# Optimization experiments

Measured on AMD Instinct MI355X. Metric: run time of the kernel, lower is better.

Reference implementation:

```python
import jax, jax.numpy as jnp
import numpy as np

N, B, T, F_IN, H1, H2 = 69, 32, 1024, 8, 32, 16


def cal_adj_norm(adj):
    # adj_norm = D^-1/2 (A + I) D^-1/2
    n = adj.shape[0]
    adj_ = adj + jnp.eye(n, dtype=adj.dtype)
    d = jnp.sum(adj_, axis=1)
    d_is = d ** -0.5
    return adj_ * d_is[:, None] * d_is[None, :]


def setup_inputs() -> dict:
    key = jax.random.key(0)
    k1, k2, k3, k4 = jax.random.split(key, 4)
    x = jax.random.normal(k1, (N, B, T, F_IN), dtype=jnp.float32)
    a = jax.random.uniform(k2, (N, N), dtype=jnp.float32)
    adj = ((a + a.T) > 1.4).astype(jnp.float32)
    W1 = jax.random.normal(k3, (F_IN, H1), dtype=jnp.float32)
    W2 = jax.random.normal(k4, (H1, H2), dtype=jnp.float32)
    return {"x": x, "adj": adj, "W1": W1, "W2": W2}


def reference(x, adj, W1, W2):
    adj_n = cal_adj_norm(adj)                      # [N, N]
    xb = jnp.transpose(x, (1, 2, 0, 3))            # [B, T, N, F_in]
    # layer 1: relu( adj_n @ x @ W1 ), batched over (B, T)
    h = jax.nn.relu(jnp.einsum('nm,btmf->btnf', adj_n, xb) @ W1)   # [B, T, N, H1]
    # layer 2: sigmoid( adj_n @ h @ W2 )
    out = jax.nn.sigmoid(jnp.einsum('nm,btmf->btnf', adj_n, h) @ W2)  # [B, T, N, H2]
    return out
```

## Files before the change

### kernel.cpp

```cpp
#include <hip/hip_runtime.h>
#include <math.h>

#define N_NODES 69
#define MP      80
#define KP      96
#define BT_TOTAL 32768
#define F_IN    8
#define H1      32
#define H2      16

#define TBT     8
#define BLOCK   256

#define XPITCH  68
#define ZPITCH  136
#define RSTRIDE 72
#define RROWS   576

typedef __attribute__((ext_vector_type(8))) short bf16x8;
typedef __attribute__((ext_vector_type(4))) float f32x4;

__device__ __forceinline__ unsigned short f2bf(float f) {
    unsigned u = __float_as_uint(f);
    return (unsigned short)((u + 0x7FFFu + ((u >> 16) & 1u)) >> 16);
}
__device__ __forceinline__ float bf2f(unsigned short h) {
    return __uint_as_float(((unsigned)h) << 16);
}

__global__ void setup_kernel(const float* __restrict__ adj,
                             const float* __restrict__ W1,
                             const float* __restrict__ W2,
                             unsigned short* __restrict__ adjh,
                             unsigned short* __restrict__ adjl,
                             unsigned short* __restrict__ W1p,
                             unsigned short* __restrict__ W2p)
{
    __shared__ float dinv[N_NODES];
    const int tid = threadIdx.x;
    if (tid < N_NODES) {
        float s = 1.0f;
        for (int j = 0; j < N_NODES; ++j) s += adj[tid * N_NODES + j];
        dinv[tid] = rsqrtf(s);
    }
    __syncthreads();
    for (int idx = tid; idx < MP * KP; idx += BLOCK) {
        const int n = idx / KP, m = idx % KP;
        float v = 0.0f;
        if (n < N_NODES && m < N_NODES) {
            float a = adj[n * N_NODES + m] + (n == m ? 1.0f : 0.0f);
            v = a * dinv[n] * dinv[m];
        }
        unsigned short h = f2bf(v);
        adjh[idx] = h;
        adjl[idx] = f2bf(v - bf2f(h));
    }
    for (int i = tid; i < 2 * 64 * F_IN; i += BLOCK) {
        const int nt = i >> 9;
        const int ln = (i >> 3) & 63;
        const int j  = i & 7;
        const int q = ln >> 4, l = ln & 15;
        float v = (q == 0) ? W1[j * H1 + nt * 16 + l] : 0.0f;
        W1p[i] = f2bf(v);
    }
    for (int i = tid; i < 64 * F_IN; i += BLOCK) {
        const int ln = i >> 3, j = i & 7;
        const int q = ln >> 4, l = ln & 15;
        W2p[i] = f2bf(W2[(q * 8 + j) * H2 + l]);
    }
}

__global__ __launch_bounds__(BLOCK, 4) void gcn_kernel(
    const float* __restrict__ x,
    const unsigned short* __restrict__ adjh,
    const unsigned short* __restrict__ adjl,
    const unsigned short* __restrict__ W1p,
    const unsigned short* __restrict__ W2p,
    float* __restrict__ out)
{
    __shared__ unsigned short U_s[KP * ZPITCH];
    __shared__ unsigned short Y1_s[RROWS * F_IN];
    __shared__ unsigned short Hb_s[4][16 * H1];

    const int tid  = threadIdx.x;
    const int lane = tid & 63;
    const int wv   = tid >> 6;
    const int quad = lane >> 4;
    const int l16  = lane & 15;
    const int bt0  = blockIdx.x * TBT;

    unsigned short* Xhi = U_s;
    unsigned short* Xlo = U_s + KP * XPITCH;

    for (int i = tid; i < N_NODES * 16; i += BLOCK) {
        const int m = i >> 4, c4 = i & 15;
        const float4 v = ((const float4*)x)[(size_t)m * (BT_TOTAL * 2) + bt0 * 2 + c4];
        unsigned short h0 = f2bf(v.x), h1 = f2bf(v.y), h2 = f2bf(v.z), h3 = f2bf(v.w);
        uint2 hi2 = make_uint2((unsigned)h0 | ((unsigned)h1 << 16),
                               (unsigned)h2 | ((unsigned)h3 << 16));
        unsigned short g0 = f2bf(v.x - bf2f(h0)), g1 = f2bf(v.y - bf2f(h1));
        unsigned short g2 = f2bf(v.z - bf2f(h2)), g3 = f2bf(v.w - bf2f(h3));
        uint2 lo2 = make_uint2((unsigned)g0 | ((unsigned)g1 << 16),
                               (unsigned)g2 | ((unsigned)g3 << 16));
        *(uint2*)((char*)Xhi + 2 * (m * XPITCH + 4 * c4)) = hi2;
        *(uint2*)((char*)Xlo + 2 * (m * XPITCH + 4 * c4)) = lo2;
    }
    for (int i = tid; i < 27 * 34; i += BLOCK) {
        const int row = N_NODES + i / 34, w = i % 34;
        ((unsigned*)Xhi)[row * 34 + w] = 0u;
        ((unsigned*)Xlo)[row * 34 + w] = 0u;
    }
    __syncthreads();

    const bf16x8 w1f0 = *(const bf16x8*)&W1p[lane * 8];
    const bf16x8 w1f1 = *(const bf16x8*)&W1p[(64 + lane) * 8];
    const bf16x8 w2f  = *(const bf16x8*)&W2p[lane * 8];

    const int ct  = wv;
    const int col = ct * 16 + l16;
    bf16x8 bh[3], bl[3];
#pragma unroll
    for (int kt = 0; kt < 3; ++kt) {
        const int k0 = kt * 32 + quad * 8;
#pragma unroll
        for (int j = 0; j < 8; ++j) {
            bh[kt][j] = (short)Xhi[(k0 + j) * XPITCH + col];
            bl[kt][j] = (short)Xlo[(k0 + j) * XPITCH + col];
        }
    }
    __syncthreads();

    for (int i = tid; i < 27 * 64; i += BLOCK) {
        const int row = N_NODES + (i >> 6), w = i & 63;
        ((unsigned*)U_s)[row * 68 + w] = 0u;
    }

    const int btc = col >> 3, fc = col & 7;
#pragma unroll
    for (int mt = 0; mt < 5; ++mt) {
        f32x4 acc = {0.f, 0.f, 0.f, 0.f};
#pragma unroll
        for (int kt = 0; kt < 3; ++kt) {
            const int aoff = (mt * 16 + l16) * KP + kt * 32 + quad * 8;
            const bf16x8 ah = *(const bf16x8*)(adjh + aoff);
            const bf16x8 al = *(const bf16x8*)(adjl + aoff);
            acc = __builtin_amdgcn_mfma_f32_16x16x32_bf16(ah, bh[kt], acc, 0, 0, 0);
            acc = __builtin_amdgcn_mfma_f32_16x16x32_bf16(ah, bl[kt], acc, 0, 0, 0);
            acc = __builtin_amdgcn_mfma_f32_16x16x32_bf16(al, bh[kt], acc, 0, 0, 0);
        }
#pragma unroll
        for (int reg = 0; reg < 4; ++reg) {
            const int n = mt * 16 + quad * 4 + reg;
            if (n < RSTRIDE)
                Y1_s[(btc * RSTRIDE + n) * F_IN + fc] = f2bf(acc[reg]);
        }
    }

    unsigned short* Hb = Hb_s[wv];
#pragma unroll
    for (int mt2 = 0; mt2 < 9; ++mt2) {
        const int rb = wv * 144 + mt2 * 16;

        bf16x8 af = {0, 0, 0, 0, 0, 0, 0, 0};
        if (quad == 0)
            af = *(const bf16x8*)&Y1_s[(rb + l16) * F_IN];

        f32x4 h0 = {0.f, 0.f, 0.f, 0.f};
        f32x4 h1 = {0.f, 0.f, 0.f, 0.f};
        h0 = __builtin_amdgcn_mfma_f32_16x16x32_bf16(af, w1f0, h0, 0, 0, 0);
        h1 = __builtin_amdgcn_mfma_f32_16x16x32_bf16(af, w1f1, h1, 0, 0, 0);

#pragma unroll
        for (int reg = 0; reg < 4; ++reg) {
            const int row = quad * 4 + reg;
            Hb[row * H1 + l16]      = f2bf(fmaxf(h0[reg], 0.f));
            Hb[row * H1 + 16 + l16] = f2bf(fmaxf(h1[reg], 0.f));
        }
        const bf16x8 a2 = *(const bf16x8*)&Hb[l16 * H1 + quad * 8];

        f32x4 zk = {0.f, 0.f, 0.f, 0.f};
        zk = __builtin_amdgcn_mfma_f32_16x16x32_bf16(a2, w2f, zk, 0, 0, 0);

#pragma unroll
        for (int reg = 0; reg < 4; ++reg) {
            const int r  = rb + quad * 4 + reg;
            const int bt = r / RSTRIDE;
            const int n  = r - bt * RSTRIDE;
            if (n < N_NODES)
                U_s[n * ZPITCH + bt * 16 + l16] = f2bf(zk[reg]);
        }
    }
    __syncthreads();

#pragma unroll
    for (int c = 0; c < 2; ++c) {
        const int ct3  = wv * 2 + c;
        const int col3 = ct3 * 16 + l16;
        bf16x8 bz[3];
#pragma unroll
        for (int kt = 0; kt < 3; ++kt) {
            const int k0 = kt * 32 + quad * 8;
#pragma unroll
            for (int j = 0; j < 8; ++j)
                bz[kt][j] = (short)U_s[(k0 + j) * ZPITCH + col3];
        }
#pragma unroll
        for (int mt = 0; mt < 5; ++mt) {
            f32x4 acc = {0.f, 0.f, 0.f, 0.f};
#pragma unroll
            for (int kt = 0; kt < 3; ++kt) {
                const bf16x8 ah =
                    *(const bf16x8*)(adjh + (mt * 16 + l16) * KP + kt * 32 + quad * 8);
                acc = __builtin_amdgcn_mfma_f32_16x16x32_bf16(ah, bz[kt], acc, 0, 0, 0);
            }
#pragma unroll
            for (int reg = 0; reg < 4; ++reg) {
                const int n = mt * 16 + quad * 4 + reg;
                if (n < N_NODES) {
                    const float v = 1.0f / (1.0f + __expf(-acc[reg]));
                    out[((size_t)(bt0 + ct3) * N_NODES + n) * H2 + l16] = v;
                }
            }
        }
    }
}

extern "C" void kernel_launch(void* const* d_in, const int* in_sizes, int n_in,
                              void* d_out, int out_size, void* d_ws, size_t ws_size,
                              hipStream_t stream) {
    const float* x   = (const float*)d_in[0];
    const float* adj = (const float*)d_in[1];
    const float* W1  = (const float*)d_in[2];
    const float* W2  = (const float*)d_in[3];
    float* out = (float*)d_out;

    unsigned short* adjh = (unsigned short*)d_ws;
    unsigned short* adjl = adjh + MP * KP;
    unsigned short* W1p  = adjl + MP * KP;
    unsigned short* W2p  = W1p + 2 * 64 * F_IN;

    setup_kernel<<<1, BLOCK, 0, stream>>>(adj, W1, W2, adjh, adjl, W1p, W2p);
    gcn_kernel<<<BT_TOTAL / TBT, BLOCK, 0, stream>>>(x, adjh, adjl, W1p, W2p, out);
}
```

Baseline: 268.9 us.

## Load x straight into MFMA A-fragments, skipping LDS staging and a barrier

The first aggregation now has each lane read x directly from global memory, split it into bf16 hi/lo parts in registers, and use it as the A operand. The normalized adjacency becomes the B operand, which transposes the MFMA roles. This removes the LDS staging of x, the gather of strided LDS columns, and two __syncthreads. The Hb scratch buffer also gets a padded pitch to reduce LDS bank conflicts. In exchange, the global loads are scalar 4-byte reads strided across nodes instead of float4 reads, and register pressure rises from five live accumulators.

```diff
diff --git a/kernel.cpp b/kernel.cpp
--- a/kernel.cpp
+++ b/kernel.cpp
@@ -12,8 +12,8 @@
 #define TBT     8
 #define BLOCK   256
 
-#define XPITCH  68
 #define ZPITCH  136
+#define HBPITCH 40
 #define RSTRIDE 72
 #define RROWS   576
 
@@ -80,7 +80,7 @@
 {
     __shared__ unsigned short U_s[KP * ZPITCH];
     __shared__ unsigned short Y1_s[RROWS * F_IN];
-    __shared__ unsigned short Hb_s[4][16 * H1];
+    __shared__ unsigned short Hb_s[4][16 * HBPITCH];
 
     const int tid  = threadIdx.x;
     const int lane = tid & 63;
@@ -89,72 +89,64 @@
     const int l16  = lane & 15;
     const int bt0  = blockIdx.x * TBT;
 
-    unsigned short* Xhi = U_s;
-    unsigned short* Xlo = U_s + KP * XPITCH;
-
-    for (int i = tid; i < N_NODES * 16; i += BLOCK) {
-        const int m = i >> 4, c4 = i & 15;
-        const float4 v = ((const float4*)x)[(size_t)m * (BT_TOTAL * 2) + bt0 * 2 + c4];
-        unsigned short h0 = f2bf(v.x), h1 = f2bf(v.y), h2 = f2bf(v.z), h3 = f2bf(v.w);
-        uint2 hi2 = make_uint2((unsigned)h0 | ((unsigned)h1 << 16),
-                               (unsigned)h2 | ((unsigned)h3 << 16));
-        unsigned short g0 = f2bf(v.x - bf2f(h0)), g1 = f2bf(v.y - bf2f(h1));
-        unsigned short g2 = f2bf(v.z - bf2f(h2)), g3 = f2bf(v.w - bf2f(h3));
-        uint2 lo2 = make_uint2((unsigned)g0 | ((unsigned)g1 << 16),
-                               (unsigned)g2 | ((unsigned)g3 << 16));
-        *(uint2*)((char*)Xhi + 2 * (m * XPITCH + 4 * c4)) = hi2;
-        *(uint2*)((char*)Xlo + 2 * (m * XPITCH + 4 * c4)) = lo2;
-    }
-    for (int i = tid; i < 27 * 34; i += BLOCK) {
-        const int row = N_NODES + i / 34, w = i % 34;
-        ((unsigned*)Xhi)[row * 34 + w] = 0u;
-        ((unsigned*)Xlo)[row * 34 + w] = 0u;
-    }
-    __syncthreads();
+    for (int i = tid; i < 27 * 64; i += BLOCK) {
+        const int row = N_NODES + (i >> 6), w = i & 63;
+        ((unsigned*)U_s)[row * 68 + w] = 0u;
+    }
+
+    const int btg = bt0 + wv * 2 + (l16 >> 3);
+    const int fl  = l16 & 7;
+
+    f32x4 acc[5] = {};
+#pragma unroll
+    for (int kt = 0; kt < 3; ++kt) {
+        union AF { unsigned u[4]; bf16x8 v; } ah, al;
+#pragma unroll
+        for (int p = 0; p < 4; ++p) {
+            const int m0 = kt * 32 + quad * 8 + 2 * p;
+            const int m1 = m0 + 1;
+            float x0 = 0.0f, x1 = 0.0f;
+            if (kt < 2) {
+                x0 = x[(size_t)m0 * 262144 + btg * 8 + fl];
+                x1 = x[(size_t)m1 * 262144 + btg * 8 + fl];
+            } else {
+                if (m0 < N_NODES) x0 = x[(size_t)m0 * 262144 + btg * 8 + fl];
+                if (m1 < N_NODES) x1 = x[(size_t)m1 * 262144 + btg * 8 + fl];
+            }
+            const unsigned short h0 = f2bf(x0), h1 = f2bf(x1);
+            ah.u[p] = (unsigned)h0 | ((unsigned)h1 << 16);
+            const unsigned short g0 = f2bf(x0 - bf2f(h0));
+            const unsigned short g1 = f2bf(x1 - bf2f(h1));
+            al.u[p] = (unsigned)g0 | ((unsigned)g1 << 16);
+        }
+#pragma unroll
+        for (int nt = 0; nt < 5; ++nt) {
+            const int boff = (nt * 16 + l16) * KP + kt * 32 + quad * 8;
+            const bf16x8 bh = *(const bf16x8*)(adjh + boff);
+            const bf16x8 bl = *(const bf16x8*)(adjl + boff);
+            acc[nt] = __builtin_amdgcn_mfma_f32_16x16x32_bf16(ah.v, bh, acc[nt], 0, 0, 0);
+            acc[nt] = __builtin_amdgcn_mfma_f32_16x16x32_bf16(ah.v, bl, acc[nt], 0, 0, 0);
+            acc[nt] = __builtin_amdgcn_mfma_f32_16x16x32_bf16(al.v, bh, acc[nt], 0, 0, 0);
+        }
+    }
+
+    {
+        const int btc = wv * 2 + (quad >> 1);
+        const int fcb = (quad & 1) * 4;
+#pragma unroll
+        for (int nt = 0; nt < 5; ++nt) {
+            const int n = nt * 16 + l16;
+            if (n < RSTRIDE) {
+#pragma unroll
+                for (int reg = 0; reg < 4; ++reg)
+                    Y1_s[(btc * RSTRIDE + n) * F_IN + fcb + reg] = f2bf(acc[nt][reg]);
+            }
+        }
+    }
 
     const bf16x8 w1f0 = *(const bf16x8*)&W1p[lane * 8];
     const bf16x8 w1f1 = *(const bf16x8*)&W1p[(64 + lane) * 8];
     const bf16x8 w2f  = *(const bf16x8*)&W2p[lane * 8];
-
-    const int ct  = wv;
-    const int col = ct * 16 + l16;
-    bf16x8 bh[3], bl[3];
-#pragma unroll
-    for (int kt = 0; kt < 3; ++kt) {
-        const int k0 = kt * 32 + quad * 8;
-#pragma unroll
-        for (int j = 0; j < 8; ++j) {
-            bh[kt][j] = (short)Xhi[(k0 + j) * XPITCH + col];
-            bl[kt][j] = (short)Xlo[(k0 + j) * XPITCH + col];
-        }
-    }
-    __syncthreads();
-
-    for (int i = tid; i < 27 * 64; i += BLOCK) {
-        const int row = N_NODES + (i >> 6), w = i & 63;
-        ((unsigned*)U_s)[row * 68 + w] = 0u;
-    }
-
-    const int btc = col >> 3, fc = col & 7;
-#pragma unroll
-    for (int mt = 0; mt < 5; ++mt) {
-        f32x4 acc = {0.f, 0.f, 0.f, 0.f};
-#pragma unroll
-        for (int kt = 0; kt < 3; ++kt) {
-            const int aoff = (mt * 16 + l16) * KP + kt * 32 + quad * 8;
-            const bf16x8 ah = *(const bf16x8*)(adjh + aoff);
-            const bf16x8 al = *(const bf16x8*)(adjl + aoff);
-            acc = __builtin_amdgcn_mfma_f32_16x16x32_bf16(ah, bh[kt], acc, 0, 0, 0);
-            acc = __builtin_amdgcn_mfma_f32_16x16x32_bf16(ah, bl[kt], acc, 0, 0, 0);
-            acc = __builtin_amdgcn_mfma_f32_16x16x32_bf16(al, bh[kt], acc, 0, 0, 0);
-        }
-#pragma unroll
-        for (int reg = 0; reg < 4; ++reg) {
-            const int n = mt * 16 + quad * 4 + reg;
-            if (n < RSTRIDE)
-                Y1_s[(btc * RSTRIDE + n) * F_IN + fc] = f2bf(acc[reg]);
-        }
-    }
 
     unsigned short* Hb = Hb_s[wv];
 #pragma unroll
@@ -173,10 +165,10 @@
 #pragma unroll
         for (int reg = 0; reg < 4; ++reg) {
             const int row = quad * 4 + reg;
-            Hb[row * H1 + l16]      = f2bf(fmaxf(h0[reg], 0.f));
-            Hb[row * H1 + 16 + l16] = f2bf(fmaxf(h1[reg], 0.f));
-        }
-        const bf16x8 a2 = *(const bf16x8*)&Hb[l16 * H1 + quad * 8];
+            Hb[row * HBPITCH + l16]      = f2bf(fmaxf(h0[reg], 0.f));
+            Hb[row * HBPITCH + 16 + l16] = f2bf(fmaxf(h1[reg], 0.f));
+        }
+        const bf16x8 a2 = *(const bf16x8*)&Hb[l16 * HBPITCH + quad * 8];
 
         f32x4 zk = {0.f, 0.f, 0.f, 0.f};
         zk = __builtin_amdgcn_mfma_f32_16x16x32_bf16(a2, w2f, zk, 0, 0, 0);
@@ -206,18 +198,18 @@
         }
 #pragma unroll
         for (int mt = 0; mt < 5; ++mt) {
-            f32x4 acc = {0.f, 0.f, 0.f, 0.f};
+            f32x4 acc3 = {0.f, 0.f, 0.f, 0.f};
 #pragma unroll
             for (int kt = 0; kt < 3; ++kt) {
                 const bf16x8 ah =
                     *(const bf16x8*)(adjh + (mt * 16 + l16) * KP + kt * 32 + quad * 8);
-                acc = __builtin_amdgcn_mfma_f32_16x16x32_bf16(ah, bz[kt], acc, 0, 0, 0);
+                acc3 = __builtin_amdgcn_mfma_f32_16x16x32_bf16(ah, bz[kt], acc3, 0, 0, 0);
             }
 #pragma unroll
             for (int reg = 0; reg < 4; ++reg) {
                 const int n = mt * 16 + quad * 4 + reg;
                 if (n < N_NODES) {
-                    const float v = 1.0f / (1.0f + __expf(-acc[reg]));
+                    const float v = 1.0f / (1.0f + __expf(-acc3[reg]));
                     out[((size_t)(bt0 + ct3) * N_NODES + n) * H2 + l16] = v;
                 }
             }
```

After: 264.6 us. Within noise of the previous version (-1.6%).
